# Kernel tuning notes

Hardware: AMD Instinct MI355X
Metric: run time of the kernel (lower is better)

Reference implementation:

```python
import jax, jax.numpy as jnp
import numpy as np

N, E, IN, HID, H, OUT = 50000, 800000, 128, 64, 2, 1
NEG_SLOPE = 0.2


def setup_inputs() -> dict:
    key = jax.random.key(0)
    ks = jax.random.split(key, 12)
    g = lambda k, shape, fi, fo: jax.random.normal(k, shape, jnp.float32) * np.sqrt(2.0 / (fi + fo)).astype(np.float32)
    x = jax.random.normal(ks[0], (N, IN), jnp.float32)
    edge_index = jax.random.randint(ks[1], (2, E), 0, N, jnp.int64)
    HC = H * HID
    W1 = g(ks[2], (HC, IN), IN, HC)
    b1 = jnp.zeros((HC,), jnp.float32)
    att1 = g(ks[3], (1, H, HID), HID, HID)
    W2 = g(ks[4], (HC, HC), HC, HC)
    b2 = jnp.zeros((HC,), jnp.float32)
    att2 = g(ks[5], (1, H, HID), HID, HID)
    Wp1 = g(ks[6], (HID, HC), HC, HID)
    bp1 = jnp.zeros((HID,), jnp.float32)
    Wp2 = g(ks[7], (OUT, HID), HID, OUT)
    bp2 = jnp.zeros((OUT,), jnp.float32)
    return {"x": x, "edge_index": edge_index, "W1": W1, "b1": b1, "att1": att1,
            "W2": W2, "b2": b2, "att2": att2, "Wp1": Wp1, "bp1": bp1, "Wp2": Wp2, "bp2": bp2}


def _segment_softmax(alpha, idx, n):
    # alpha: [E, H]; softmax over edges sharing the same destination node
    m = jax.ops.segment_max(alpha, idx, num_segments=n)
    m = jnp.where(jnp.isfinite(m), m, 0.0)  # empty segments -> -inf guard
    ex = jnp.exp(alpha - m[idx])
    s = jax.ops.segment_sum(ex, idx, num_segments=n)
    return ex / (s[idx] + 1e-16)


def _gatv2(x, edge_index, W, b, att):
    n = x.shape[0]
    h, c = att.shape[1], att.shape[2]
    xw = (x @ W.T + b).reshape(n, h, c)          # shared lin_l == lin_r
    src, dst = edge_index[0], edge_index[1]       # x_j = xw[src], x_i = xw[dst]
    xj = xw[src]                                  # [E, H, C]
    e = jax.nn.leaky_relu(xw[dst] + xj, NEG_SLOPE)
    alpha = jnp.einsum('ehc,ohc->eh', e, att)     # [E, H]
    alpha = _segment_softmax(alpha, dst, n)
    msg = xj * alpha[:, :, None]                  # message uses x_j (not e)
    out = jax.ops.segment_sum(msg, dst, num_segments=n)
    return out.reshape(n, h * c)


def reference(x, edge_index, W1, b1, att1, W2, b2, att2, Wp1, bp1, Wp2, bp2):
    # eval mode: dropout is identity
    h = jax.nn.relu(_gatv2(x, edge_index, W1, b1, att1))
    h = jax.nn.relu(_gatv2(h, edge_index, W2, b2, att2))
    h = h @ Wp1.T + bp1
    h = h @ Wp2.T + bp2
    return jax.nn.sigmoid(h)
```

## Files before the change

### kernel.cpp

```cpp
#include <hip/hip_runtime.h>
#include <math.h>

typedef __attribute__((ext_vector_type(2))) float f32x2;
typedef __attribute__((ext_vector_type(4))) float fx4;
typedef __attribute__((ext_vector_type(8))) short s16x8;

#define SUBK 8


__global__ void zero_k(int4* __restrict__ p, int n4){
  int i = blockIdx.x*blockDim.x + threadIdx.x;
  if(i < n4) p[i] = make_int4(0,0,0,0);
}


__global__ void scan1_k(const int* __restrict__ cnt, int* __restrict__ bsum, int n){
  __shared__ int ws[16];
  int i = blockIdx.x*1024 + threadIdx.x;
  int v = (i < n) ? cnt[i] : 0;
  #pragma unroll
  for(int m=1;m<64;m<<=1) v += __shfl_xor(v, m);
  if((threadIdx.x & 63) == 0) ws[threadIdx.x >> 6] = v;
  __syncthreads();
  if(threadIdx.x == 0){
    int s = 0;
    #pragma unroll
    for(int w=0; w<16; w++) s += ws[w];
    bsum[blockIdx.x] = s;
  }
}

__global__ __launch_bounds__(1024) void scan2_k(int* __restrict__ bsum, int nb,
                                                int* __restrict__ bin_ptr, int nbins, int E){
  __shared__ int sm[1024];
  int t = threadIdx.x;
  int v = (t < nb) ? bsum[t] : 0;
  sm[t] = v;
  __syncthreads();
  for(int off=1; off<1024; off<<=1){
    int tv = (t>=off)? sm[t-off] : 0;
    __syncthreads();
    sm[t] += tv;
    __syncthreads();
  }
  if(t < nb) bsum[t] = sm[t] - v;
  if(t == 0) bin_ptr[nbins] = E;
}

__global__ void scan3_k(const int* __restrict__ cnt, const int* __restrict__ bsum,
                        int* __restrict__ bin_ptr, int n){
  __shared__ int sm[1024];
  int i = blockIdx.x*1024 + threadIdx.x;
  int v = (i<n)? cnt[i] : 0;
  sm[threadIdx.x] = v;
  __syncthreads();
  for(int off=1; off<1024; off<<=1){
    int t = (threadIdx.x>=off)? sm[threadIdx.x-off] : 0;
    __syncthreads();
    sm[threadIdx.x] += t;
    __syncthreads();
  }
  if(i<n)
    bin_ptr[i] = sm[threadIdx.x] - v + bsum[blockIdx.x];
}

__global__ void fill2_k(const int* __restrict__ src, const int* __restrict__ dst,
                        const int* __restrict__ slot, const int* __restrict__ bin_ptr,
                        int* __restrict__ csr_src, int E){
  int e = blockIdx.x*blockDim.x + threadIdx.x;
  if(e < E){
    int bin = dst[e]*SUBK + (e & (SUBK-1));
    csr_src[bin_ptr[bin] + slot[e]] = src[e];
  }
}


__device__ __forceinline__ unsigned pack_bf2(float lo, float hi){
  unsigned ul = __float_as_uint(lo); ul += 0x7fffu + ((ul>>16)&1u);
  unsigned uh = __float_as_uint(hi); uh += 0x7fffu + ((uh>>16)&1u);
  return (uh & 0xffff0000u) | (ul >> 16);
}


__device__ __forceinline__ void gemm_core(uint4* Wl, const float* __restrict__ X,
    const float* __restrict__ b, unsigned short* __restrict__ Ybf, int nrows, int brow, int t)
{
  int wv = t >> 6, lane = t & 63;
  int r = lane & 15, kb = lane >> 4;
  int row = brow*64 + wv*16 + r;
  const float* xrow = &X[(size_t)min(row, nrows-1)*128];

  fx4 acc[8];
  #pragma unroll
  for(int c=0;c<8;c++) acc[c] = (fx4){0.f,0.f,0.f,0.f};

  #pragma unroll
  for(int kt=0;kt<4;kt++){
    int k0 = kt*32 + kb*8;
    float4 v0 = *(const float4*)&xrow[k0];
    float4 v1 = *(const float4*)&xrow[k0+4];
    float vs[8] = {v0.x,v0.y,v0.z,v0.w,v1.x,v1.y,v1.z,v1.w};
    s16x8 ahi, alo;
    #pragma unroll
    for(int j=0;j<8;j++){
      unsigned u = __float_as_uint(vs[j]);
      unsigned uh = u + 0x7fffu + ((u>>16)&1u);
      unsigned short h = (unsigned short)(uh >> 16);
      float hf = __uint_as_float(((unsigned)h)<<16);
      float lo = vs[j] - hf;
      unsigned ul = __float_as_uint(lo);
      ul += 0x7fffu + ((ul>>16)&1u);
      ahi[j] = (short)h;
      alo[j] = (short)(ul>>16);
    }
    int chunk = kt*4 + kb;
    #pragma unroll
    for(int c=0;c<8;c++){
      uint4 wb = Wl[((c*16 + r)<<4) | (chunk ^ r)];
      s16x8 bb = *(s16x8*)&wb;
      acc[c] = __builtin_amdgcn_mfma_f32_16x16x32_bf16(ahi, bb, acc[c], 0,0,0);
      acc[c] = __builtin_amdgcn_mfma_f32_16x16x32_bf16(alo, bb, acc[c], 0,0,0);
    }
  }

  __syncthreads();
  unsigned short* lds = (unsigned short*)Wl;
  unsigned short* my = lds + wv*2048;
  int colb = lane & 15;
  int rq0 = (lane>>4)*4;
  #pragma unroll
  for(int c=0;c<8;c++){
    int col = c*16 + colb;
    float bias = b[col];
    #pragma unroll
    for(int q=0;q<4;q++){
      unsigned u = __float_as_uint(acc[c][q] + bias);
      u += 0x7fffu + ((u>>16)&1u);
      my[(rq0+q)*128 + col] = (unsigned short)(u>>16);
    }
  }
  const uint4* my4 = (const uint4*)my;
  uint4* Y4 = (uint4*)Ybf;
  #pragma unroll
  for(int rr=0;rr<4;rr++){
    int idx = lane + 64*rr;
    int lrow = idx >> 4, lcol = idx & 15;
    int grow = brow*64 + wv*16 + lrow;
    if(grow < nrows)
      Y4[(size_t)grow*16 + lcol] = my4[idx];
  }
}


__global__ __launch_bounds__(256) void prep_gemm1_k(
    const float* __restrict__ X, const float* __restrict__ W1, const float* __restrict__ b1,
    unsigned short* __restrict__ XWbf, int nrows, int nGB,
    const int* __restrict__ dst, int* __restrict__ cnt, int* __restrict__ slot, int E, int nAB,
    const float* __restrict__ W2, unsigned short* __restrict__ W2bf,
    const float* __restrict__ Wp1, const float* __restrict__ bp1,
    const float* __restrict__ Wp2, const float* __restrict__ bp2,
    float* __restrict__ wfold)
{
  __shared__ uint4 Wl[128*16];
  int b = blockIdx.x;
  int t = threadIdx.x;

  if(b < nGB){
    #pragma unroll
    for(int i=0;i<8;i++){
      int idx = t + i*256;
      int row = idx >> 4, ch = idx & 15;
      const float* wsrc = &W1[(size_t)row*128 + ch*8];
      float4 va = *(const float4*)&wsrc[0];
      float4 vb = *(const float4*)&wsrc[4];
      uint4 o;
      o.x = pack_bf2(va.x, va.y); o.y = pack_bf2(va.z, va.w);
      o.z = pack_bf2(vb.x, vb.y); o.w = pack_bf2(vb.z, vb.w);
      Wl[(row<<4) | (ch ^ (row & 15))] = o;
    }
    __syncthreads();
    gemm_core(Wl, X, b1, XWbf, nrows, b, t);
    return;
  }
  int ab = b - nGB;
  if(ab < nAB){
    const int STR = nAB*256;
    int base = ab*256 + t;
    int e = base;
    for(; e + 3*STR < E; e += 4*STR){
      int e1 = e+STR, e2 = e+2*STR, e3 = e+3*STR;
      int d0 = dst[e], d1 = dst[e1], d2 = dst[e2], d3 = dst[e3];
      int s0 = atomicAdd(&cnt[d0*SUBK + (e &(SUBK-1))], 1);
      int s1 = atomicAdd(&cnt[d1*SUBK + (e1&(SUBK-1))], 1);
      int s2 = atomicAdd(&cnt[d2*SUBK + (e2&(SUBK-1))], 1);
      int s3 = atomicAdd(&cnt[d3*SUBK + (e3&(SUBK-1))], 1);
      slot[e] = s0; slot[e1] = s1; slot[e2] = s2; slot[e3] = s3;
    }
    for(; e < E; e += STR){
      int d = dst[e];
      slot[e] = atomicAdd(&cnt[d*SUBK + (e&(SUBK-1))], 1);
    }
    return;
  }
  int tb = ab - nAB;
  if(tb == 0){
    const float4* Ws = (const float4*)W2;
    uint2* Wd = (uint2*)W2bf;
    #pragma unroll
    for(int i=0;i<16;i++){
      int idx = t + i*256;
      float4 v = Ws[idx];
      uint2 o; o.x = pack_bf2(v.x, v.y); o.y = pack_bf2(v.z, v.w);
      Wd[idx] = o;
    }
    return;
  }
  int k = t;
  if(k < 128){
    float s = 0.f;
    for(int j=0;j<64;j++) s += Wp2[j]*Wp1[(size_t)j*128 + k];
    wfold[k] = s;
  } else if(k == 128){
    float s = bp2[0];
    for(int j=0;j<64;j++) s += Wp2[j]*bp1[j];
    wfold[128] = s;
  }
}


__global__ __launch_bounds__(256) void gemm_mfma_k(
    const float* __restrict__ X, const unsigned short* __restrict__ Wbf,
    const float* __restrict__ b, unsigned short* __restrict__ Ybf, int nrows)
{
  __shared__ uint4 Wl[128*16];
  int t = threadIdx.x;
  {
    const uint4* Ws = (const uint4*)Wbf;
    #pragma unroll
    for(int i=0;i<8;i++){
      int idx = t + i*256;
      int row = idx >> 4, ch = idx & 15;
      Wl[(row<<4) | (ch ^ (row & 15))] = Ws[idx];
    }
  }
  __syncthreads();
  gemm_core(Wl, X, b, Ybf, nrows, blockIdx.x, t);
}


#define BFLO(u) __uint_as_float((u)<<16)
#define BFHI(u) __uint_as_float((u)&0xffff0000u)
#define DPP_ADD(v, ctrl) { int _t = __builtin_amdgcn_update_dpp(0, __float_as_int(v), ctrl, 0xF, 0xF, true); (v) += __int_as_float(_t); }

template<int FUSE>
__global__ __launch_bounds__(256) void gat_v4_k(
    const unsigned short* __restrict__ XWbf,
    const float* __restrict__ att,
    const int* __restrict__ bin_ptr, const int* __restrict__ csr_src,
    float* __restrict__ outp, const float* __restrict__ wfold, int n)
{
  int wid = threadIdx.x >> 6, lane = threadIdx.x & 63;
  int node = blockIdx.x*4 + wid;
  if(node >= n) return;
  int g = lane >> 4;
  int cg = lane & 15;
  int c8 = cg * 8;

  float4 A0 = *(const float4*)&att[c8];
  float4 A1 = *(const float4*)&att[c8+4];
  f32x2 a[4] = { {A0.x,A0.y}, {A0.z,A0.w}, {A1.x,A1.y}, {A1.z,A1.w} };

  const uint4* XW4 = (const uint4*)XWbf;
  uint4 du = XW4[(size_t)node*16 + cg];
  f32x2 xd[4] = { {BFLO(du.x),BFHI(du.x)}, {BFLO(du.y),BFHI(du.y)},
                  {BFLO(du.z),BFHI(du.z)}, {BFLO(du.w),BFHI(du.w)} };

  int beg = bin_ptr[node*SUBK], end = bin_ptr[node*SUBK + SUBK];
  float s = 0.f;
  f32x2 acc[4] = {{0.f,0.f},{0.f,0.f},{0.f,0.f},{0.f,0.f}};

  if(end > beg){
    int sn_cur = csr_src[min(beg + g, end-1)];
    int sn_nxt = (beg+4 < end) ? csr_src[min(beg+4 + g, end-1)] : sn_cur;
    uint4 u = XW4[(size_t)sn_cur*16 + cg];
    for(int i = beg; i < end; i += 4){
      uint4 u_nxt = XW4[(size_t)sn_nxt*16 + cg];
      int sn_nn = (i+8 < end) ? csr_src[min(i+8 + g, end-1)] : sn_nxt;
      bool ok = (i + g) < end;

      f32x2 x0 = {BFLO(u.x), BFHI(u.x)};
      f32x2 x1 = {BFLO(u.y), BFHI(u.y)};
      f32x2 x2 = {BFLO(u.z), BFHI(u.z)};
      f32x2 x3 = {BFLO(u.w), BFHI(u.w)};
      f32x2 v0 = xd[0]+x0, v1 = xd[1]+x1, v2 = xd[2]+x2, v3 = xd[3]+x3;
      f32x2 q0 = v0*0.2f, q1 = v1*0.2f, q2 = v2*0.2f, q3 = v3*0.2f;
      f32x2 l0, l1, l2, l3;
      l0.x = fmaxf(v0.x,q0.x); l0.y = fmaxf(v0.y,q0.y);
      l1.x = fmaxf(v1.x,q1.x); l1.y = fmaxf(v1.y,q1.y);
      l2.x = fmaxf(v2.x,q2.x); l2.y = fmaxf(v2.y,q2.y);
      l3.x = fmaxf(v3.x,q3.x); l3.y = fmaxf(v3.y,q3.y);
      f32x2 p2 = l0*a[0];
      p2 += l1*a[1];
      p2 += l2*a[2];
      p2 += l3*a[3];
      float p = p2.x + p2.y;
      DPP_ADD(p, 0xB1);
      DPP_ADD(p, 0x4E);
      DPP_ADD(p, 0x141);
      float ex = ok ? __expf(fminf(p, 60.f)) : 0.f;
      s += ex;
      f32x2 e2 = {ex, ex};
      acc[0] += e2*x0;
      acc[1] += e2*x1;
      acc[2] += e2*x2;
      acc[3] += e2*x3;

      u = u_nxt; sn_nxt = sn_nn;
    }
  }

  s += __shfl_xor(s,16);  s += __shfl_xor(s,32);
  #pragma unroll
  for(int j=0;j<4;j++){
    acc[j].x += __shfl_xor(acc[j].x,16); acc[j].x += __shfl_xor(acc[j].x,32);
    acc[j].y += __shfl_xor(acc[j].y,16); acc[j].y += __shfl_xor(acc[j].y,32);
  }

  float inv = (s > 0.f) ? 1.f/s : 0.f;
  f32x2 o[4];
  #pragma unroll
  for(int j=0;j<4;j++){
    o[j].x = fmaxf(acc[j].x*inv, 0.f);
    o[j].y = fmaxf(acc[j].y*inv, 0.f);
  }

  if(FUSE == 0){
    if(lane < 16){
      *(float4*)&outp[(size_t)node*128 + c8]     = make_float4(o[0].x,o[0].y,o[1].x,o[1].y);
      *(float4*)&outp[(size_t)node*128 + c8 + 4] = make_float4(o[2].x,o[2].y,o[3].x,o[3].y);
    }
  } else {
    float4 wf0 = *(const float4*)&wfold[c8];
    float4 wf1 = *(const float4*)&wfold[c8+4];
    float tt = o[0].x*wf0.x + o[0].y*wf0.y + o[1].x*wf0.z + o[1].y*wf0.w
             + o[2].x*wf1.x + o[2].y*wf1.y + o[3].x*wf1.z + o[3].y*wf1.w;
    DPP_ADD(tt, 0xB1);
    DPP_ADD(tt, 0x4E);
    DPP_ADD(tt, 0x141);
    DPP_ADD(tt, 0x140);
    if(lane == 0)
      outp[node] = 1.f/(1.f + __expf(-(tt + wfold[128])));
  }
}


static inline size_t alignup(size_t v){ return (v + 255) & ~(size_t)255; }

extern "C" void kernel_launch(void* const* d_in, const int* in_sizes, int n_in,
                              void* d_out, int out_size, void* d_ws, size_t ws_size,
                              hipStream_t stream) {
  const float* x    = (const float*)d_in[0];
  const int*   ei   = (const int*)  d_in[1];
  const float* W1   = (const float*)d_in[2];
  const float* b1   = (const float*)d_in[3];
  const float* att1 = (const float*)d_in[4];
  const float* W2   = (const float*)d_in[5];
  const float* b2   = (const float*)d_in[6];
  const float* att2 = (const float*)d_in[7];
  const float* Wp1  = (const float*)d_in[8];
  const float* bp1  = (const float*)d_in[9];
  const float* Wp2  = (const float*)d_in[10];
  const float* bp2  = (const float*)d_in[11];
  float* out = (float*)d_out;

  int N = in_sizes[0] / 128;
  int E = in_sizes[1] / 2;
  int nbins = N * SUBK;

  char* ws = (char*)d_ws;
  size_t off = 0;
  float* G1            = (float*)(ws + off); off = alignup(off + (size_t)N*128*sizeof(float));
  unsigned short* XWbf = (unsigned short*)(ws + off); off = alignup(off + (size_t)N*128*sizeof(unsigned short));
  int* csr_src  = (int*)(ws + off); off = alignup(off + (size_t)E*sizeof(int));
  int* slot     = (int*)(ws + off); off = alignup(off + (size_t)E*sizeof(int));
  int* bin_ptr  = (int*)(ws + off); off = alignup(off + (size_t)(nbins+1)*sizeof(int));
  int* cnt      = (int*)(ws + off); off = alignup(off + (size_t)(nbins+4)*sizeof(int));
  int* bsum     = (int*)(ws + off); off = alignup(off + 1024*sizeof(int));
  unsigned short* W2bf = (unsigned short*)(ws + off); off = alignup(off + 128*128*sizeof(unsigned short));
  float* wfold  = (float*)(ws + off); off = alignup(off + 129*sizeof(float));

  const int* esrc = ei;
  const int* edst = ei + E;

  int n4 = (nbins + 3) / 4;
  zero_k<<<(n4 + 255)/256, 256, 0, stream>>>((int4*)cnt, n4);

  int nGB = (N + 63) / 64;
  int nAB = 256;
  int nb = (nbins + 1023) / 1024;

  prep_gemm1_k<<<nGB + nAB + 2, 256, 0, stream>>>(
      x, W1, b1, XWbf, N, nGB,
      edst, cnt, slot, E, nAB,
      W2, W2bf, Wp1, bp1, Wp2, bp2, wfold);

  scan1_k<<<nb, 1024, 0, stream>>>(cnt, bsum, nbins);
  scan2_k<<<1, 1024, 0, stream>>>(bsum, nb, bin_ptr, nbins, E);
  scan3_k<<<nb, 1024, 0, stream>>>(cnt, bsum, bin_ptr, nbins);
  fill2_k<<<(E+255)/256, 256, 0, stream>>>(esrc, edst, slot, bin_ptr, csr_src, E);

  gat_v4_k<0><<<(N+3)/4, 256, 0, stream>>>(XWbf, att1, bin_ptr, csr_src, G1, nullptr, N);
  gemm_mfma_k<<<nGB, 256, 0, stream>>>(G1, W2bf, b2, XWbf, N);
  gat_v4_k<1><<<(N+3)/4, 256, 0, stream>>>(XWbf, att2, bin_ptr, csr_src, out, wfold, N);
}
```

Baseline: 150.9 us.

## Map one node per 16-lane group and drop sub-binned CSR counters

The GAT aggregation kernel now assigns one destination node to each 16-lane quarter-wave, so each wave handles four nodes that walk their edge lists serially. Previously a whole wave handled one node and split its edges across four groups. Because the edge split inside a node is gone, the 8-way sub-binned counters used to build the CSR are replaced by one counter per node. That shrinks the count array and the scans, but increases atomic contention on popular destination nodes. The trade-off is fewer cross-lane reductions and less wasted lane work on low-degree nodes, at the cost of divergent loop lengths within a wave and a longer serial dependency chain per node.

```diff
diff --git a/kernel.cpp b/kernel.cpp
--- a/kernel.cpp
+++ b/kernel.cpp
@@ -4,8 +4,6 @@
 typedef __attribute__((ext_vector_type(2))) float f32x2;
 typedef __attribute__((ext_vector_type(4))) float fx4;
 typedef __attribute__((ext_vector_type(8))) short s16x8;
-
-#define SUBK 8
 
 
 __global__ void zero_k(int4* __restrict__ p, int n4){
@@ -31,7 +29,7 @@
 }
 
 __global__ __launch_bounds__(1024) void scan2_k(int* __restrict__ bsum, int nb,
-                                                int* __restrict__ bin_ptr, int nbins, int E){
+                                                int* __restrict__ row_ptr, int n, int E){
   __shared__ int sm[1024];
   int t = threadIdx.x;
   int v = (t < nb) ? bsum[t] : 0;
@@ -44,11 +42,11 @@
     __syncthreads();
   }
   if(t < nb) bsum[t] = sm[t] - v;
-  if(t == 0) bin_ptr[nbins] = E;
+  if(t == 0) row_ptr[n] = E;
 }
 
 __global__ void scan3_k(const int* __restrict__ cnt, const int* __restrict__ bsum,
-                        int* __restrict__ bin_ptr, int n){
+                        int* __restrict__ row_ptr, int n){
   __shared__ int sm[1024];
   int i = blockIdx.x*1024 + threadIdx.x;
   int v = (i<n)? cnt[i] : 0;
@@ -61,17 +59,15 @@
     __syncthreads();
   }
   if(i<n)
-    bin_ptr[i] = sm[threadIdx.x] - v + bsum[blockIdx.x];
+    row_ptr[i] = sm[threadIdx.x] - v + bsum[blockIdx.x];
 }
 
 __global__ void fill2_k(const int* __restrict__ src, const int* __restrict__ dst,
-                        const int* __restrict__ slot, const int* __restrict__ bin_ptr,
+                        const int* __restrict__ slot, const int* __restrict__ row_ptr,
                         int* __restrict__ csr_src, int E){
   int e = blockIdx.x*blockDim.x + threadIdx.x;
-  if(e < E){
-    int bin = dst[e]*SUBK + (e & (SUBK-1));
-    csr_src[bin_ptr[bin] + slot[e]] = src[e];
-  }
+  if(e < E)
+    csr_src[row_ptr[dst[e]] + slot[e]] = src[e];
 }
 
 
@@ -185,21 +181,18 @@
   int ab = b - nGB;
   if(ab < nAB){
     const int STR = nAB*256;
-    int base = ab*256 + t;
-    int e = base;
+    int e = ab*256 + t;
     for(; e + 3*STR < E; e += 4*STR){
       int e1 = e+STR, e2 = e+2*STR, e3 = e+3*STR;
       int d0 = dst[e], d1 = dst[e1], d2 = dst[e2], d3 = dst[e3];
-      int s0 = atomicAdd(&cnt[d0*SUBK + (e &(SUBK-1))], 1);
-      int s1 = atomicAdd(&cnt[d1*SUBK + (e1&(SUBK-1))], 1);
-      int s2 = atomicAdd(&cnt[d2*SUBK + (e2&(SUBK-1))], 1);
-      int s3 = atomicAdd(&cnt[d3*SUBK + (e3&(SUBK-1))], 1);
+      int s0 = atomicAdd(&cnt[d0], 1);
+      int s1 = atomicAdd(&cnt[d1], 1);
+      int s2 = atomicAdd(&cnt[d2], 1);
+      int s3 = atomicAdd(&cnt[d3], 1);
       slot[e] = s0; slot[e1] = s1; slot[e2] = s2; slot[e3] = s3;
     }
-    for(; e < E; e += STR){
-      int d = dst[e];
-      slot[e] = atomicAdd(&cnt[d*SUBK + (e&(SUBK-1))], 1);
-    }
+    for(; e < E; e += STR)
+      slot[e] = atomicAdd(&cnt[dst[e]], 1);
     return;
   }
   int tb = ab - nAB;
@@ -253,77 +246,79 @@
 #define DPP_ADD(v, ctrl) { int _t = __builtin_amdgcn_update_dpp(0, __float_as_int(v), ctrl, 0xF, 0xF, true); (v) += __int_as_float(_t); }
 
 template<int FUSE>
-__global__ __launch_bounds__(256) void gat_v4_k(
+__global__ __launch_bounds__(256) void gat_v6_k(
     const unsigned short* __restrict__ XWbf,
     const float* __restrict__ att,
-    const int* __restrict__ bin_ptr, const int* __restrict__ csr_src,
+    const int* __restrict__ row_ptr, const int* __restrict__ csr_src,
     float* __restrict__ outp, const float* __restrict__ wfold, int n)
 {
   int wid = threadIdx.x >> 6, lane = threadIdx.x & 63;
-  int node = blockIdx.x*4 + wid;
-  if(node >= n) return;
   int g = lane >> 4;
   int cg = lane & 15;
   int c8 = cg * 8;
+  int node = blockIdx.x*16 + wid*4 + g;
+  bool nv = node < n;
+  int nodec = nv ? node : (n-1);
 
   float4 A0 = *(const float4*)&att[c8];
   float4 A1 = *(const float4*)&att[c8+4];
   f32x2 a[4] = { {A0.x,A0.y}, {A0.z,A0.w}, {A1.x,A1.y}, {A1.z,A1.w} };
 
   const uint4* XW4 = (const uint4*)XWbf;
-  uint4 du = XW4[(size_t)node*16 + cg];
+  uint4 du = XW4[(size_t)nodec*16 + cg];
   f32x2 xd[4] = { {BFLO(du.x),BFHI(du.x)}, {BFLO(du.y),BFHI(du.y)},
                   {BFLO(du.z),BFHI(du.z)}, {BFLO(du.w),BFHI(du.w)} };
 
-  int beg = bin_ptr[node*SUBK], end = bin_ptr[node*SUBK + SUBK];
+  int beg = nv ? row_ptr[nodec]   : 0;
+  int end = nv ? row_ptr[nodec+1] : 0;
+
   float s = 0.f;
   f32x2 acc[4] = {{0.f,0.f},{0.f,0.f},{0.f,0.f},{0.f,0.f}};
 
-  if(end > beg){
-    int sn_cur = csr_src[min(beg + g, end-1)];
-    int sn_nxt = (beg+4 < end) ? csr_src[min(beg+4 + g, end-1)] : sn_cur;
-    uint4 u = XW4[(size_t)sn_cur*16 + cg];
-    for(int i = beg; i < end; i += 4){
-      uint4 u_nxt = XW4[(size_t)sn_nxt*16 + cg];
-      int sn_nn = (i+8 < end) ? csr_src[min(i+8 + g, end-1)] : sn_nxt;
-      bool ok = (i + g) < end;
-
-      f32x2 x0 = {BFLO(u.x), BFHI(u.x)};
-      f32x2 x1 = {BFLO(u.y), BFHI(u.y)};
-      f32x2 x2 = {BFLO(u.z), BFHI(u.z)};
-      f32x2 x3 = {BFLO(u.w), BFHI(u.w)};
-      f32x2 v0 = xd[0]+x0, v1 = xd[1]+x1, v2 = xd[2]+x2, v3 = xd[3]+x3;
-      f32x2 q0 = v0*0.2f, q1 = v1*0.2f, q2 = v2*0.2f, q3 = v3*0.2f;
-      f32x2 l0, l1, l2, l3;
-      l0.x = fmaxf(v0.x,q0.x); l0.y = fmaxf(v0.y,q0.y);
-      l1.x = fmaxf(v1.x,q1.x); l1.y = fmaxf(v1.y,q1.y);
-      l2.x = fmaxf(v2.x,q2.x); l2.y = fmaxf(v2.y,q2.y);
-      l3.x = fmaxf(v3.x,q3.x); l3.y = fmaxf(v3.y,q3.y);
-      f32x2 p2 = l0*a[0];
-      p2 += l1*a[1];
-      p2 += l2*a[2];
-      p2 += l3*a[3];
-      float p = p2.x + p2.y;
-      DPP_ADD(p, 0xB1);
-      DPP_ADD(p, 0x4E);
-      DPP_ADD(p, 0x141);
-      float ex = ok ? __expf(fminf(p, 60.f)) : 0.f;
-      s += ex;
-      f32x2 e2 = {ex, ex};
-      acc[0] += e2*x0;
-      acc[1] += e2*x1;
-      acc[2] += e2*x2;
-      acc[3] += e2*x3;
-
-      u = u_nxt; sn_nxt = sn_nn;
-    }
-  }
-
-  s += __shfl_xor(s,16);  s += __shfl_xor(s,32);
-  #pragma unroll
-  for(int j=0;j<4;j++){
-    acc[j].x += __shfl_xor(acc[j].x,16); acc[j].x += __shfl_xor(acc[j].x,32);
-    acc[j].y += __shfl_xor(acc[j].y,16); acc[j].y += __shfl_xor(acc[j].y,32);
+  int e = beg;
+  int sn1 = 0;
+  uint4 u = {0u,0u,0u,0u};
+  if(e < end){
+    int sn0 = csr_src[e];
+    u = XW4[(size_t)sn0*16 + cg];
+  }
+  if(e+1 < end) sn1 = csr_src[e+1];
+
+  while(__any(e < end)){
+    bool ok  = e < end;
+    bool okn = (e+1) < end;
+    uint4 un = u;
+    if(okn) un = XW4[(size_t)sn1*16 + cg];
+    int sn2 = ((e+2) < end) ? csr_src[e+2] : sn1;
+
+    f32x2 x0 = {BFLO(u.x), BFHI(u.x)};
+    f32x2 x1 = {BFLO(u.y), BFHI(u.y)};
+    f32x2 x2 = {BFLO(u.z), BFHI(u.z)};
+    f32x2 x3 = {BFLO(u.w), BFHI(u.w)};
+    f32x2 v0 = xd[0]+x0, v1 = xd[1]+x1, v2 = xd[2]+x2, v3 = xd[3]+x3;
+    f32x2 q0 = v0*0.2f, q1 = v1*0.2f, q2 = v2*0.2f, q3 = v3*0.2f;
+    f32x2 l0, l1, l2, l3;
+    l0.x = fmaxf(v0.x,q0.x); l0.y = fmaxf(v0.y,q0.y);
+    l1.x = fmaxf(v1.x,q1.x); l1.y = fmaxf(v1.y,q1.y);
+    l2.x = fmaxf(v2.x,q2.x); l2.y = fmaxf(v2.y,q2.y);
+    l3.x = fmaxf(v3.x,q3.x); l3.y = fmaxf(v3.y,q3.y);
+    f32x2 p2 = l0*a[0];
+    p2 += l1*a[1];
+    p2 += l2*a[2];
+    p2 += l3*a[3];
+    float p = p2.x + p2.y;
+    DPP_ADD(p, 0xB1);
+    DPP_ADD(p, 0x4E);
+    DPP_ADD(p, 0x141);
+    float ex = ok ? __expf(fminf(p, 60.f)) : 0.f;
+    s += ex;
+    f32x2 e2 = {ex, ex};
+    acc[0] += e2*x0;
+    acc[1] += e2*x1;
+    acc[2] += e2*x2;
+    acc[3] += e2*x3;
+
+    u = un; sn1 = sn2; e = e + 1;
   }
 
   float inv = (s > 0.f) ? 1.f/s : 0.f;
@@ -335,7 +330,7 @@
   }
 
   if(FUSE == 0){
-    if(lane < 16){
+    if(nv){
       *(float4*)&outp[(size_t)node*128 + c8]     = make_float4(o[0].x,o[0].y,o[1].x,o[1].y);
       *(float4*)&outp[(size_t)node*128 + c8 + 4] = make_float4(o[2].x,o[2].y,o[3].x,o[3].y);
     }
@@ -348,7 +343,7 @@
     DPP_ADD(tt, 0x4E);
     DPP_ADD(tt, 0x141);
     DPP_ADD(tt, 0x140);
-    if(lane == 0)
+    if(cg == 0 && nv)
       outp[node] = 1.f/(1.f + __expf(-(tt + wfold[128])));
   }
 }
@@ -375,7 +370,6 @@
 
   int N = in_sizes[0] / 128;
   int E = in_sizes[1] / 2;
-  int nbins = N * SUBK;
 
   char* ws = (char*)d_ws;
   size_t off = 0;
@@ -383,8 +377,8 @@
   unsigned short* XWbf = (unsigned short*)(ws + off); off = alignup(off + (size_t)N*128*sizeof(unsigned short));
   int* csr_src  = (int*)(ws + off); off = alignup(off + (size_t)E*sizeof(int));
   int* slot     = (int*)(ws + off); off = alignup(off + (size_t)E*sizeof(int));
-  int* bin_ptr  = (int*)(ws + off); off = alignup(off + (size_t)(nbins+1)*sizeof(int));
-  int* cnt      = (int*)(ws + off); off = alignup(off + (size_t)(nbins+4)*sizeof(int));
+  int* row_ptr  = (int*)(ws + off); off = alignup(off + (size_t)(N+1)*sizeof(int));
+  int* cnt      = (int*)(ws + off); off = alignup(off + (size_t)(N+4)*sizeof(int));
   int* bsum     = (int*)(ws + off); off = alignup(off + 1024*sizeof(int));
   unsigned short* W2bf = (unsigned short*)(ws + off); off = alignup(off + 128*128*sizeof(unsigned short));
   float* wfold  = (float*)(ws + off); off = alignup(off + 129*sizeof(float));
@@ -392,24 +386,25 @@
   const int* esrc = ei;
   const int* edst = ei + E;
 
-  int n4 = (nbins + 3) / 4;
+  int n4 = (N + 3) / 4;
   zero_k<<<(n4 + 255)/256, 256, 0, stream>>>((int4*)cnt, n4);
 
   int nGB = (N + 63) / 64;
   int nAB = 256;
-  int nb = (nbins + 1023) / 1024;
+  int nb = (N + 1023) / 1024;
 
   prep_gemm1_k<<<nGB + nAB + 2, 256, 0, stream>>>(
       x, W1, b1, XWbf, N, nGB,
       edst, cnt, slot, E, nAB,
       W2, W2bf, Wp1, bp1, Wp2, bp2, wfold);
 
-  scan1_k<<<nb, 1024, 0, stream>>>(cnt, bsum, nbins);
-  scan2_k<<<1, 1024, 0, stream>>>(bsum, nb, bin_ptr, nbins, E);
-  scan3_k<<<nb, 1024, 0, stream>>>(cnt, bsum, bin_ptr, nbins);
-  fill2_k<<<(E+255)/256, 256, 0, stream>>>(esrc, edst, slot, bin_ptr, csr_src, E);
-
-  gat_v4_k<0><<<(N+3)/4, 256, 0, stream>>>(XWbf, att1, bin_ptr, csr_src, G1, nullptr, N);
+  scan1_k<<<nb, 1024, 0, stream>>>(cnt, bsum, N);
+  scan2_k<<<1, 1024, 0, stream>>>(bsum, nb, row_ptr, N, E);
+  scan3_k<<<nb, 1024, 0, stream>>>(cnt, bsum, row_ptr, N);
+  fill2_k<<<(E+255)/256, 256, 0, stream>>>(esrc, edst, slot, row_ptr, csr_src, E);
+
+  int gatB = (N + 15) / 16;
+  gat_v6_k<0><<<gatB, 256, 0, stream>>>(XWbf, att1, row_ptr, csr_src, G1, nullptr, N);
   gemm_mfma_k<<<nGB, 256, 0, stream>>>(G1, W2bf, b2, XWbf, N);
-  gat_v4_k<1><<<(N+3)/4, 256, 0, stream>>>(XWbf, att2, bin_ptr, csr_src, out, wfold, N);
-}
+  gat_v6_k<1><<<gatB, 256, 0, stream>>>(XWbf, att2, row_ptr, csr_src, out, wfold, N);
+}
```

New measurement: 155.3 us. +3.0%, slower.

## Build CSR via LDS-local histograms per node range and edge chunk

Applied to the files above, without the earlier changes.

Replaces the global-atomic counting sort (8 sub-bins per node, a per-edge slot array, and a zeroing kernel) with a two-level scheme. Each block histograms one edge chunk restricted to one node range, using LDS atomics, and writes 16-bit per-chunk counts. A scan produces per-node row pointers and per-chunk offsets, and a fill kernel scatters src ids using LDS cursors. This removes global atomic contention and the slot buffer. In exchange, each edge chunk is re-read once per node range (4 ranges), the fill kernel uses a large LDS allocation, and the 16-bit counts assume small per-chunk degrees.

```diff
diff --git a/kernel.cpp b/kernel.cpp
--- a/kernel.cpp
+++ b/kernel.cpp
@@ -5,74 +5,8 @@
 typedef __attribute__((ext_vector_type(4))) float fx4;
 typedef __attribute__((ext_vector_type(8))) short s16x8;
 
-#define SUBK 8
-
-
-__global__ void zero_k(int4* __restrict__ p, int n4){
-  int i = blockIdx.x*blockDim.x + threadIdx.x;
-  if(i < n4) p[i] = make_int4(0,0,0,0);
-}
-
-
-__global__ void scan1_k(const int* __restrict__ cnt, int* __restrict__ bsum, int n){
-  __shared__ int ws[16];
-  int i = blockIdx.x*1024 + threadIdx.x;
-  int v = (i < n) ? cnt[i] : 0;
-  #pragma unroll
-  for(int m=1;m<64;m<<=1) v += __shfl_xor(v, m);
-  if((threadIdx.x & 63) == 0) ws[threadIdx.x >> 6] = v;
-  __syncthreads();
-  if(threadIdx.x == 0){
-    int s = 0;
-    #pragma unroll
-    for(int w=0; w<16; w++) s += ws[w];
-    bsum[blockIdx.x] = s;
-  }
-}
-
-__global__ __launch_bounds__(1024) void scan2_k(int* __restrict__ bsum, int nb,
-                                                int* __restrict__ bin_ptr, int nbins, int E){
-  __shared__ int sm[1024];
-  int t = threadIdx.x;
-  int v = (t < nb) ? bsum[t] : 0;
-  sm[t] = v;
-  __syncthreads();
-  for(int off=1; off<1024; off<<=1){
-    int tv = (t>=off)? sm[t-off] : 0;
-    __syncthreads();
-    sm[t] += tv;
-    __syncthreads();
-  }
-  if(t < nb) bsum[t] = sm[t] - v;
-  if(t == 0) bin_ptr[nbins] = E;
-}
-
-__global__ void scan3_k(const int* __restrict__ cnt, const int* __restrict__ bsum,
-                        int* __restrict__ bin_ptr, int n){
-  __shared__ int sm[1024];
-  int i = blockIdx.x*1024 + threadIdx.x;
-  int v = (i<n)? cnt[i] : 0;
-  sm[threadIdx.x] = v;
-  __syncthreads();
-  for(int off=1; off<1024; off<<=1){
-    int t = (threadIdx.x>=off)? sm[threadIdx.x-off] : 0;
-    __syncthreads();
-    sm[threadIdx.x] += t;
-    __syncthreads();
-  }
-  if(i<n)
-    bin_ptr[i] = sm[threadIdx.x] - v + bsum[blockIdx.x];
-}
-
-__global__ void fill2_k(const int* __restrict__ src, const int* __restrict__ dst,
-                        const int* __restrict__ slot, const int* __restrict__ bin_ptr,
-                        int* __restrict__ csr_src, int E){
-  int e = blockIdx.x*blockDim.x + threadIdx.x;
-  if(e < E){
-    int bin = dst[e]*SUBK + (e & (SUBK-1));
-    csr_src[bin_ptr[bin] + slot[e]] = src[e];
-  }
-}
+#define EC 32
+#define RRN 12500
 
 
 __device__ __forceinline__ unsigned pack_bf2(float lo, float hi){
@@ -152,20 +86,22 @@
 }
 
 
-__global__ __launch_bounds__(256) void prep_gemm1_k(
+__global__ __launch_bounds__(256) void mega_k(
     const float* __restrict__ X, const float* __restrict__ W1, const float* __restrict__ b1,
     unsigned short* __restrict__ XWbf, int nrows, int nGB,
-    const int* __restrict__ dst, int* __restrict__ cnt, int* __restrict__ slot, int E, int nAB,
+    const int* __restrict__ dst, int E, int CH, int NR,
+    unsigned short* __restrict__ cnt16, int N,
     const float* __restrict__ W2, unsigned short* __restrict__ W2bf,
     const float* __restrict__ Wp1, const float* __restrict__ bp1,
     const float* __restrict__ Wp2, const float* __restrict__ bp2,
     float* __restrict__ wfold)
 {
-  __shared__ uint4 Wl[128*16];
+  __shared__ int smem[RRN + 300];
   int b = blockIdx.x;
   int t = threadIdx.x;
 
   if(b < nGB){
+    uint4* Wl = (uint4*)smem;
     #pragma unroll
     for(int i=0;i<8;i++){
       int idx = t + i*256;
@@ -182,27 +118,24 @@
     gemm_core(Wl, X, b1, XWbf, nrows, b, t);
     return;
   }
-  int ab = b - nGB;
-  if(ab < nAB){
-    const int STR = nAB*256;
-    int base = ab*256 + t;
-    int e = base;
-    for(; e + 3*STR < E; e += 4*STR){
-      int e1 = e+STR, e2 = e+2*STR, e3 = e+3*STR;
-      int d0 = dst[e], d1 = dst[e1], d2 = dst[e2], d3 = dst[e3];
-      int s0 = atomicAdd(&cnt[d0*SUBK + (e &(SUBK-1))], 1);
-      int s1 = atomicAdd(&cnt[d1*SUBK + (e1&(SUBK-1))], 1);
-      int s2 = atomicAdd(&cnt[d2*SUBK + (e2&(SUBK-1))], 1);
-      int s3 = atomicAdd(&cnt[d3*SUBK + (e3&(SUBK-1))], 1);
-      slot[e] = s0; slot[e1] = s1; slot[e2] = s2; slot[e3] = s3;
-    }
-    for(; e < E; e += STR){
+  int hb = b - nGB;
+  if(hb < NR*EC){
+    int r = hb >> 5, c = hb & (EC-1);
+    int r0 = r*RRN, rend = min(r0+RRN, N);
+    int rn = rend - r0;
+    for(int d=t; d<rn; d+=256) smem[d] = 0;
+    __syncthreads();
+    int e0 = c*CH, e1 = min(e0+CH, E);
+    for(int e = e0+t; e < e1; e += 256){
       int d = dst[e];
-      slot[e] = atomicAdd(&cnt[d*SUBK + (e&(SUBK-1))], 1);
-    }
+      if(d >= r0 && d < rend) atomicAdd(&smem[d-r0], 1);
+    }
+    __syncthreads();
+    unsigned short* outp = cnt16 + (size_t)c*N;
+    for(int d=t; d<rn; d+=256) outp[r0+d] = (unsigned short)smem[d];
     return;
   }
-  int tb = ab - nAB;
+  int tb = hb - NR*EC;
   if(tb == 0){
     const float4* Ws = (const float4*)W2;
     uint2* Wd = (uint2*)W2bf;
@@ -228,6 +161,94 @@
 }
 
 
+__global__ __launch_bounds__(1024) void scan1_k(const unsigned short* __restrict__ cnt16,
+    unsigned short* __restrict__ offs16, int* __restrict__ total,
+    int* __restrict__ bsum, int n){
+  __shared__ int ws[16];
+  int i = blockIdx.x*1024 + threadIdx.x;
+  int v = 0;
+  if(i < n){
+    int s = 0;
+    #pragma unroll
+    for(int c=0;c<EC;c++){
+      int tc = cnt16[(size_t)c*n + i];
+      offs16[(size_t)c*n + i] = (unsigned short)s;
+      s += tc;
+    }
+    total[i] = s;
+    v = s;
+  }
+  #pragma unroll
+  for(int m=1;m<64;m<<=1) v += __shfl_xor(v, m);
+  if((threadIdx.x & 63) == 0) ws[threadIdx.x >> 6] = v;
+  __syncthreads();
+  if(threadIdx.x == 0){
+    int s = 0;
+    #pragma unroll
+    for(int w=0; w<16; w++) s += ws[w];
+    bsum[blockIdx.x] = s;
+  }
+}
+
+__global__ __launch_bounds__(1024) void scan2_k(int* __restrict__ bsum, int nb,
+                                                int* __restrict__ row_ptr, int n, int E){
+  __shared__ int sm[1024];
+  int t = threadIdx.x;
+  int v = (t < nb) ? bsum[t] : 0;
+  sm[t] = v;
+  __syncthreads();
+  for(int off=1; off<1024; off<<=1){
+    int tv = (t>=off)? sm[t-off] : 0;
+    __syncthreads();
+    sm[t] += tv;
+    __syncthreads();
+  }
+  if(t < nb) bsum[t] = sm[t] - v;
+  if(t == 0) row_ptr[n] = E;
+}
+
+__global__ void scan3_k(const int* __restrict__ total, const int* __restrict__ bsum,
+                        int* __restrict__ row_ptr, int n){
+  __shared__ int sm[1024];
+  int i = blockIdx.x*1024 + threadIdx.x;
+  int v = (i<n)? total[i] : 0;
+  sm[threadIdx.x] = v;
+  __syncthreads();
+  for(int off=1; off<1024; off<<=1){
+    int t = (threadIdx.x>=off)? sm[threadIdx.x-off] : 0;
+    __syncthreads();
+    sm[threadIdx.x] += t;
+    __syncthreads();
+  }
+  if(i<n)
+    row_ptr[i] = sm[threadIdx.x] - v + bsum[blockIdx.x];
+}
+
+
+__global__ __launch_bounds__(256) void fillC_k(
+    const int* __restrict__ src, const int* __restrict__ dst,
+    const unsigned short* __restrict__ offs16, const int* __restrict__ row_ptr,
+    int* __restrict__ csr_src, int E, int CH, int N)
+{
+  __shared__ int cursor[RRN];
+  int b = blockIdx.x, t = threadIdx.x;
+  int r = b >> 5, c = b & (EC-1);
+  int r0 = r*RRN, rend = min(r0+RRN, N);
+  int rn = rend - r0;
+  for(int d=t; d<rn; d+=256)
+    cursor[d] = row_ptr[r0+d] + (int)offs16[(size_t)c*N + r0 + d];
+  __syncthreads();
+  int e0 = c*CH, e1 = min(e0+CH, E);
+  for(int e = e0+t; e < e1; e += 256){
+    int d = dst[e];
+    if(d >= r0 && d < rend){
+      int pos = atomicAdd(&cursor[d-r0], 1);
+      csr_src[pos] = src[e];
+    }
+  }
+}
+
+
 __global__ __launch_bounds__(256) void gemm_mfma_k(
     const float* __restrict__ X, const unsigned short* __restrict__ Wbf,
     const float* __restrict__ b, unsigned short* __restrict__ Ybf, int nrows)
@@ -256,7 +277,7 @@
 __global__ __launch_bounds__(256) void gat_v4_k(
     const unsigned short* __restrict__ XWbf,
     const float* __restrict__ att,
-    const int* __restrict__ bin_ptr, const int* __restrict__ csr_src,
+    const int* __restrict__ row_ptr, const int* __restrict__ csr_src,
     float* __restrict__ outp, const float* __restrict__ wfold, int n)
 {
   int wid = threadIdx.x >> 6, lane = threadIdx.x & 63;
@@ -275,7 +296,7 @@
   f32x2 xd[4] = { {BFLO(du.x),BFHI(du.x)}, {BFLO(du.y),BFHI(du.y)},
                   {BFLO(du.z),BFHI(du.z)}, {BFLO(du.w),BFHI(du.w)} };
 
-  int beg = bin_ptr[node*SUBK], end = bin_ptr[node*SUBK + SUBK];
+  int beg = row_ptr[node], end = row_ptr[node+1];
   float s = 0.f;
   f32x2 acc[4] = {{0.f,0.f},{0.f,0.f},{0.f,0.f},{0.f,0.f}};
 
@@ -375,16 +396,18 @@
 
   int N = in_sizes[0] / 128;
   int E = in_sizes[1] / 2;
-  int nbins = N * SUBK;
+  int CH = (E + EC - 1) / EC;
+  int NR = (N + RRN - 1) / RRN;
 
   char* ws = (char*)d_ws;
   size_t off = 0;
   float* G1            = (float*)(ws + off); off = alignup(off + (size_t)N*128*sizeof(float));
   unsigned short* XWbf = (unsigned short*)(ws + off); off = alignup(off + (size_t)N*128*sizeof(unsigned short));
   int* csr_src  = (int*)(ws + off); off = alignup(off + (size_t)E*sizeof(int));
-  int* slot     = (int*)(ws + off); off = alignup(off + (size_t)E*sizeof(int));
-  int* bin_ptr  = (int*)(ws + off); off = alignup(off + (size_t)(nbins+1)*sizeof(int));
-  int* cnt      = (int*)(ws + off); off = alignup(off + (size_t)(nbins+4)*sizeof(int));
+  unsigned short* cnt16  = (unsigned short*)(ws + off); off = alignup(off + (size_t)EC*N*sizeof(unsigned short));
+  unsigned short* offs16 = (unsigned short*)(ws + off); off = alignup(off + (size_t)EC*N*sizeof(unsigned short));
+  int* row_ptr  = (int*)(ws + off); off = alignup(off + (size_t)(N+1)*sizeof(int));
+  int* total    = (int*)(ws + off); off = alignup(off + (size_t)N*sizeof(int));
   int* bsum     = (int*)(ws + off); off = alignup(off + 1024*sizeof(int));
   unsigned short* W2bf = (unsigned short*)(ws + off); off = alignup(off + 128*128*sizeof(unsigned short));
   float* wfold  = (float*)(ws + off); off = alignup(off + 129*sizeof(float));
@@ -392,24 +415,20 @@
   const int* esrc = ei;
   const int* edst = ei + E;
 
-  int n4 = (nbins + 3) / 4;
-  zero_k<<<(n4 + 255)/256, 256, 0, stream>>>((int4*)cnt, n4);
-
   int nGB = (N + 63) / 64;
-  int nAB = 256;
-  int nb = (nbins + 1023) / 1024;
-
-  prep_gemm1_k<<<nGB + nAB + 2, 256, 0, stream>>>(
+  int nb = (N + 1023) / 1024;
+
+  mega_k<<<nGB + NR*EC + 2, 256, 0, stream>>>(
       x, W1, b1, XWbf, N, nGB,
-      edst, cnt, slot, E, nAB,
+      edst, E, CH, NR, cnt16, N,
       W2, W2bf, Wp1, bp1, Wp2, bp2, wfold);
 
-  scan1_k<<<nb, 1024, 0, stream>>>(cnt, bsum, nbins);
-  scan2_k<<<1, 1024, 0, stream>>>(bsum, nb, bin_ptr, nbins, E);
-  scan3_k<<<nb, 1024, 0, stream>>>(cnt, bsum, bin_ptr, nbins);
-  fill2_k<<<(E+255)/256, 256, 0, stream>>>(esrc, edst, slot, bin_ptr, csr_src, E);
-
-  gat_v4_k<0><<<(N+3)/4, 256, 0, stream>>>(XWbf, att1, bin_ptr, csr_src, G1, nullptr, N);
+  scan1_k<<<nb, 1024, 0, stream>>>(cnt16, offs16, total, bsum, N);
+  scan2_k<<<1, 1024, 0, stream>>>(bsum, nb, row_ptr, N, E);
+  scan3_k<<<nb, 1024, 0, stream>>>(total, bsum, row_ptr, N);
+  fillC_k<<<NR*EC, 256, 0, stream>>>(esrc, edst, offs16, row_ptr, csr_src, E, CH, N);
+
+  gat_v4_k<0><<<(N+3)/4, 256, 0, stream>>>(XWbf, att1, row_ptr, csr_src, G1, nullptr, N);
   gemm_mfma_k<<<nGB, 256, 0, stream>>>(G1, W2bf, b2, XWbf, N);
-  gat_v4_k<1><<<(N+3)/4, 256, 0, stream>>>(XWbf, att2, bin_ptr, csr_src, out, wfold, N);
-}
+  gat_v4_k<1><<<(N+3)/4, 256, 0, stream>>>(XWbf, att2, row_ptr, csr_src, out, wfold, N);
+}
```

After: 191.6 us. 27.0% more time.
